# Optimization experiments

Measured on AMD Instinct MI355X. Metric: run time of the kernel, lower is better.

The kernel has to match this reference:

```python
import jax, jax.numpy as jnp
import numpy as np

B, L, H = 2, 2048, 1024
NH, HD = 16, 64          # num_heads, head_dim (NH*HD == qkv_features == H)
M = 1024                 # memory_size
SCALES = (1, 2, 4)
EPS = 1e-6


def setup_inputs() -> dict:
    key = jax.random.key(0)
    ks = jax.random.split(key, 16)
    n = lambda k, shape: (jax.random.normal(k, shape) * 0.02).astype(jnp.float32)
    return {
        "x": jax.random.normal(ks[0], (B, L, H), dtype=jnp.float32),
        "error_memory": n(ks[1], (M, H)),
        "Wq": n(ks[2], (3, H, H)), "bq": jnp.zeros((3, H), jnp.float32),
        "Wk": n(ks[3], (3, H, H)), "bk": jnp.zeros((3, H), jnp.float32),
        "Wv": n(ks[4], (3, H, H)), "bv": jnp.zeros((3, H), jnp.float32),
        "Wo": n(ks[5], (3, H, H)), "bo": jnp.zeros((3, H), jnp.float32),
        "W1": n(ks[6], (4 * H, H)), "b1": jnp.zeros((H,), jnp.float32),
        "ln_scale": jnp.ones((H,), jnp.float32),
        "ln_bias": jnp.zeros((H,), jnp.float32),
        "W2": n(ks[7], (H, H)), "b2": jnp.zeros((H,), jnp.float32),
    }


def _mha(xs, Wq, bq, Wk, bk, Wv, bv, Wo, bo):
    # flax MultiHeadDotProductAttention (self-attention, deterministic)
    Bs, S, _ = xs.shape
    q = (xs @ Wq + bq).reshape(Bs, S, NH, HD)
    k = (xs @ Wk + bk).reshape(Bs, S, NH, HD)
    v = (xs @ Wv + bv).reshape(Bs, S, NH, HD)
    att = jax.nn.softmax(
        jnp.einsum('bqhd,bkhd->bhqk', q, k) / np.sqrt(HD).astype(np.float32),
        axis=-1)
    ctx = jnp.einsum('bhqk,bkhd->bqhd', att, v).reshape(Bs, S, NH * HD)
    return ctx @ Wo + bo


def reference(x, error_memory, Wq, bq, Wk, bk, Wv, bv, Wo, bo,
              W1, b1, ln_scale, ln_bias, W2, b2):
    # multi-scale self-attention error scores
    scores = []
    for i, s in enumerate(SCALES):
        sx = x.reshape(B, L // s, s, H).mean(axis=2)
        scores.append(_mha(sx, Wq[i], bq[i], Wk[i], bk[i], Wv[i], bv[i], Wo[i], bo[i]))
    error_features = jnp.concatenate(
        [jnp.repeat(sc, s, axis=1)[:, :L, :] for sc, s in zip(scores, SCALES)],
        axis=-1)  # [B, L, 3H]

    # memory similarity softmax (detect_errors) + memory readback
    sim = jnp.einsum('blh,mh->blm', x, error_memory) / jnp.sqrt(jnp.float32(H))
    memory_weights = jax.nn.softmax(sim, axis=-1)          # [B, L, M]
    memory_context = jnp.einsum('blm,mh->blh', memory_weights, error_memory)

    cf = jnp.concatenate([error_features, memory_context], axis=-1) @ W1 + b1
    mu = cf.mean(axis=-1, keepdims=True)
    var = jnp.mean((cf - mu) ** 2, axis=-1, keepdims=True)
    cf = (cf - mu) / jnp.sqrt(var + EPS) * ln_scale + ln_bias
    cf = jax.nn.relu(cf)

    error_gate = jax.nn.sigmoid(x @ W2 + b2)
    confidence = error_gate.mean(axis=-1, keepdims=True)
    scale = jnp.sqrt(1.0 / (H * confidence + EPS))
    corrected = x + scale * error_gate * cf
    return corrected, error_gate
```

## Files before the change

kernel.cpp:

```cpp
#include <hip/hip_runtime.h>
#include <stdint.h>


#define MiBc ((size_t)1 << 20)

using s16x8 = __attribute__((ext_vector_type(8))) short;
using s16x4 = __attribute__((ext_vector_type(4))) short;
using u16x4 = __attribute__((ext_vector_type(4))) unsigned short;
using f32x4 = __attribute__((ext_vector_type(4))) float;

__device__ __forceinline__ uint16_t f2bf(float f) {
  uint32_t u = __float_as_uint(f);
  return (uint16_t)((u + 0x7fffu + ((u >> 16) & 1u)) >> 16);
}

__device__ __forceinline__ float fexp2(float x) {
  return __builtin_amdgcn_exp2f(x);
}

__device__ __forceinline__ void load_lds16(const uint16_t* g, uint16_t* l) {
  __builtin_amdgcn_global_load_lds(
      (const __attribute__((address_space(1))) void*)(const void*)g,
      (__attribute__((address_space(3))) void*)(void*)l, 16, 0, 0);
}

struct TD { const float* in; uint16_t* out; };
struct TD14 { TD d[14]; };

__global__ __launch_bounds__(256) void k_transpose(TD14 ds, int R, int C) {
  const float* in = ds.d[blockIdx.y].in;
  uint16_t* out = ds.d[blockIdx.y].out;
  const int nTC = C >> 5;
  const int bi = blockIdx.x / nTC, bj = blockIdx.x % nTC;
  __shared__ float t[32][33];
  const int tx = threadIdx.x & 31, ty = threadIdx.x >> 5;
#pragma unroll
  for (int p = 0; p < 4; ++p) {
    int r = bi * 32 + ty + p * 8;
    t[ty + p * 8][tx] = in[(size_t)r * C + bj * 32 + tx];
  }
  __syncthreads();
#pragma unroll
  for (int p = 0; p < 4; ++p) {
    int c = bj * 32 + ty + p * 8;
    out[(size_t)c * R + bi * 32 + tx] = f2bf(t[tx][ty + p * 8]);
  }
}

__global__ __launch_bounds__(256) void k_f2bf4(const float* __restrict__ in,
                                               uint16_t* __restrict__ out) {
  int i = (blockIdx.x * 256 + threadIdx.x) * 4;
  float4 v = *(const float4*)(in + i);
  u16x4 o = {f2bf(v.x), f2bf(v.y), f2bf(v.z), f2bf(v.w)};
  *(u16x4*)(out + i) = o;
}

__global__ __launch_bounds__(256) void k_biaspack(const float* __restrict__ bq,
                                                  const float* __restrict__ bk,
                                                  const float* __restrict__ bv,
                                                  float* __restrict__ dst) {
  int g = blockIdx.x * 256 + threadIdx.x;
  int i = g / 3072, j = g - i * 3072;
  const float* src = (j < 1024)   ? bq + i * 1024 + j
                     : (j < 2048) ? bk + i * 1024 + (j - 1024)
                                  : bv + i * 1024 + (j - 2048);
  dst[g] = *src;
}

__global__ __launch_bounds__(256) void k_down(const float* __restrict__ x,
                                              uint16_t* __restrict__ x1,
                                              uint16_t* __restrict__ x2,
                                              uint16_t* __restrict__ x4) {
  int g = blockIdx.x * 256 + threadIdx.x;
  int c = g & 1023;
  int l4 = (g >> 10) & 511;
  int b = g >> 19;
  const float* xp = x + (size_t)(b * 2048 + l4 * 4) * 1024 + c;
  float a0 = xp[0], a1 = xp[1024], a2 = xp[2048], a3 = xp[3072];
  size_t r1 = (size_t)(b * 2048 + l4 * 4) * 1024 + c;
  x1[r1] = f2bf(a0);
  x1[r1 + 1024] = f2bf(a1);
  x1[r1 + 2048] = f2bf(a2);
  x1[r1 + 3072] = f2bf(a3);
  size_t r2 = (size_t)(b * 1024 + l4 * 2) * 1024 + c;
  x2[r2] = f2bf(0.5f * (a0 + a1));
  x2[r2 + 1024] = f2bf(0.5f * (a2 + a3));
  x4[(size_t)(b * 512 + l4) * 1024 + c] = f2bf(0.25f * (a0 + a1 + a2 + a3));
}

__global__ __launch_bounds__(256) void k_gemm(
    const uint16_t* __restrict__ A, const uint16_t* __restrict__ BT,
    const float* __restrict__ bias, void* __restrict__ C, int M, int N, int K,
    int ldc, float scale, float qscale, int qcols, int out_bf16) {
  __shared__ __align__(16) uint16_t Al[128 * 32];
  __shared__ __align__(16) uint16_t Bl[128 * 32];
  const int tid = threadIdx.x;
  const int wave = tid >> 6, lane = tid & 63;
  const int wr = wave >> 1, wc = wave & 1;
  const int lr = lane & 15, lg = lane >> 4;
  const int bM = blockIdx.y * 128, bN = blockIdx.x * 128;
  (void)M; (void)N;

  f32x4 acc[4][4] = {};

  for (int k0 = 0; k0 < K; k0 += 32) {
    __syncthreads();
#pragma unroll
    for (int j = 0; j < 2; ++j) {
      int ck = wave * 2 + j;
      int p = ck * 64 + lane;
      int row = p >> 2, kq = p & 3;
      load_lds16(A + (size_t)(bM + row) * K + k0 + kq * 8, &Al[ck * 512]);
      load_lds16(BT + (size_t)(bN + row) * K + k0 + kq * 8, &Bl[ck * 512]);
    }
    __syncthreads();
    s16x8 af[4], bfr[4];
#pragma unroll
    for (int i = 0; i < 4; ++i)
      af[i] = *(const s16x8*)&Al[(wr * 64 + i * 16 + lr) * 32 + lg * 8];
#pragma unroll
    for (int i = 0; i < 4; ++i)
      bfr[i] = *(const s16x8*)&Bl[(wc * 64 + i * 16 + lr) * 32 + lg * 8];
#pragma unroll
    for (int i = 0; i < 4; ++i)
#pragma unroll
      for (int jn = 0; jn < 4; ++jn)
        acc[i][jn] = __builtin_amdgcn_mfma_f32_16x16x32_bf16(
            af[i], bfr[jn], acc[i][jn], 0, 0, 0);
  }

#pragma unroll
  for (int i = 0; i < 4; ++i) {
    int rg = bM + wr * 64 + i * 16 + lg * 4;
#pragma unroll
    for (int jn = 0; jn < 4; ++jn) {
      int cg = bN + wc * 64 + jn * 16 + lr;
      float bv = bias ? bias[cg] : 0.f;
      float post = (cg < qcols) ? qscale : 1.f;
#pragma unroll
      for (int r = 0; r < 4; ++r) {
        float v = (acc[i][jn][r] * scale + bv) * post;
        if (out_bf16)
          ((uint16_t*)C)[(size_t)(rg + r) * ldc + cg] = f2bf(v);
        else
          ((float*)C)[(size_t)(rg + r) * ldc + cg] = v;
      }
    }
  }
}

__global__ __launch_bounds__(256) void k_vtrans(const uint16_t* __restrict__ v,
                                                uint16_t* __restrict__ vt,
                                                int S, int ld) {
  const int nKT = S >> 6;
  const int bh = blockIdx.x / nKT, kt = blockIdx.x % nKT;
  const int b = bh >> 4, h = bh & 15;
  __shared__ uint16_t t[64][65];
  for (int i = threadIdx.x; i < 4096; i += 256) {
    int kk = i >> 6, dd = i & 63;
    t[dd][kk] = v[(size_t)(b * S + kt * 64 + kk) * ld + h * 64 + dd];
  }
  __syncthreads();
  for (int i = threadIdx.x; i < 4096; i += 256) {
    int dd = i >> 6, kk = i & 63;
    vt[((size_t)(bh * 64) + dd) * S + kt * 64 + kk] = t[dd][kk];
  }
}

__global__ __launch_bounds__(256) void k_attn(const uint16_t* __restrict__ qkv,
                                              const uint16_t* __restrict__ vt,
                                              uint16_t* __restrict__ ctx,
                                              int S) {
  const int wid = blockIdx.x * 4 + (threadIdx.x >> 6);
  const int lane = threadIdx.x & 63;
  const int nQB = S >> 5;
  const int qb = wid % nQB;
  const int bh = wid / nQB;
  const int h = bh & 15, b = bh >> 4;
  const int lr = lane & 15, lg = lane >> 4;

  const uint16_t* qp =
      qkv + (size_t)(b * S + qb * 32 + lr) * 3072 + h * 64 + lg * 8;
  s16x8 qf0[2], qf1[2];
  qf0[0] = *(const s16x8*)qp;
  qf1[0] = *(const s16x8*)(qp + 32);
  qf0[1] = *(const s16x8*)(qp + 16 * 3072);
  qf1[1] = *(const s16x8*)(qp + 16 * 3072 + 32);
  const uint16_t* kbase =
      qkv + (size_t)(b * S) * 3072 + 1024 + h * 64 + lg * 8;
  const uint16_t* vbase = vt + (size_t)(bh * 64) * S + lg * 4;

  f32x4 acc[2][4] = {};
  float mS[2] = {-1e30f, -1e30f};
  float lS[2] = {0.f, 0.f};

#define LOADK(T, K0, K1)                                               \
  {                                                                    \
    const uint16_t* kp = kbase + (size_t)((T)*16 + lr) * 3072;         \
    K0 = *(const s16x8*)kp;                                            \
    K1 = *(const s16x8*)(kp + 32);                                     \
  }
#define LOADV(T, VF)                                                   \
  {                                                                    \
    _Pragma("unroll") for (int c = 0; c < 4; ++c) VF[c] =              \
        *(const s16x4*)(vbase + (size_t)(c * 16 + lr) * S + (T)*16);   \
  }

  auto compute = [&](s16x8 K0, s16x8 K1, const s16x4 (&VF)[4]) {
#pragma unroll
    for (int f = 0; f < 2; ++f) {
      f32x4 st = {};
      st = __builtin_amdgcn_mfma_f32_16x16x32_bf16(K0, qf0[f], st, 0, 0, 0);
      st = __builtin_amdgcn_mfma_f32_16x16x32_bf16(K1, qf1[f], st, 0, 0, 0);
      float tmax = fmaxf(fmaxf(st[0], st[1]), fmaxf(st[2], st[3]));
      tmax = fmaxf(tmax, __shfl_xor(tmax, 16));
      tmax = fmaxf(tmax, __shfl_xor(tmax, 32));
      if (!__all(tmax <= mS[f])) {
        float mn = fmaxf(mS[f], tmax);
        float fac = fexp2(mS[f] - mn);
        mS[f] = mn;
        lS[f] *= fac;
#pragma unroll
        for (int c = 0; c < 4; ++c) acc[f][c] *= fac;
      }
      float p0 = fexp2(st[0] - mS[f]), p1 = fexp2(st[1] - mS[f]);
      float p2 = fexp2(st[2] - mS[f]), p3 = fexp2(st[3] - mS[f]);
      lS[f] += (p0 + p1) + (p2 + p3);
      s16x4 pb;
      pb[0] = (short)f2bf(p0);
      pb[1] = (short)f2bf(p1);
      pb[2] = (short)f2bf(p2);
      pb[3] = (short)f2bf(p3);
#pragma unroll
      for (int c = 0; c < 4; ++c)
        acc[f][c] = __builtin_amdgcn_mfma_f32_16x16x16bf16_1k(VF[c], pb,
                                                              acc[f][c], 0, 0, 0);
    }
  };

  s16x8 ka0, ka1, kb0, kb1;
  s16x4 va[4], vb[4];
  const int nT = S >> 4;
  LOADK(0, ka0, ka1);
  LOADV(0, va);
  LOADK(1, kb0, kb1);
  LOADV(1, vb);
  for (int t = 0; t < nT; t += 2) {
    compute(ka0, ka1, va);
    if (t + 2 < nT) { LOADK(t + 2, ka0, ka1); LOADV(t + 2, va); }
    compute(kb0, kb1, vb);
    if (t + 3 < nT) { LOADK(t + 3, kb0, kb1); LOADV(t + 3, vb); }
  }
#undef LOADK
#undef LOADV

#pragma unroll
  for (int f = 0; f < 2; ++f) {
    float l = lS[f];
    l += __shfl_xor(l, 16);
    l += __shfl_xor(l, 32);
    const float inv = 1.f / l;
    uint16_t* crow =
        ctx + (size_t)(b * S + qb * 32 + f * 16 + lr) * 1024 + h * 64;
#pragma unroll
    for (int c = 0; c < 4; ++c) {
      u16x4 o;
#pragma unroll
      for (int r = 0; r < 4; ++r) o[r] = f2bf(acc[f][c][r] * inv);
      *(u16x4*)(crow + c * 16 + lg * 4) = o;
    }
  }
}

__global__ __launch_bounds__(256) void k_softmax(const float* __restrict__ sim,
                                                 uint16_t* __restrict__ w) {
  __shared__ float red[4];
  const int row = blockIdx.x, t = threadIdx.x;
  const size_t base = (size_t)row * 1024 + t * 4;
  float4 v = *(const float4*)(sim + base);
  float mx = fmaxf(fmaxf(v.x, v.y), fmaxf(v.z, v.w));
#pragma unroll
  for (int o = 32; o > 0; o >>= 1) mx = fmaxf(mx, __shfl_xor(mx, o));
  if ((t & 63) == 0) red[t >> 6] = mx;
  __syncthreads();
  mx = fmaxf(fmaxf(red[0], red[1]), fmaxf(red[2], red[3]));
  __syncthreads();
  float p0 = __expf(v.x - mx), p1 = __expf(v.y - mx);
  float p2 = __expf(v.z - mx), p3 = __expf(v.w - mx);
  float s = p0 + p1 + p2 + p3;
#pragma unroll
  for (int o = 32; o > 0; o >>= 1) s += __shfl_xor(s, o);
  if ((t & 63) == 0) red[t >> 6] = s;
  __syncthreads();
  s = red[0] + red[1] + red[2] + red[3];
  float inv = 1.f / s;
  u16x4 o = {f2bf(p0 * inv), f2bf(p1 * inv), f2bf(p2 * inv), f2bf(p3 * inv)};
  *(u16x4*)(w + base) = o;
}

__global__ __launch_bounds__(256) void k_upsample(const uint16_t* __restrict__ s2,
                                                  const uint16_t* __restrict__ s4,
                                                  uint16_t* __restrict__ acf) {
  int g = blockIdx.x * 256 + threadIdx.x;
  int cg = g & 255;
  int row = g >> 8;
  int b = row >> 11, l = row & 2047;
  int c = cg * 8;
  const uint16_t* src =
      (c < 1024) ? s2 + (size_t)(b * 1024 + (l >> 1)) * 1024 + c
                 : s4 + (size_t)(b * 512 + (l >> 2)) * 1024 + (c - 1024);
  *(s16x8*)(acf + (size_t)row * 4096 + 1024 + c) = *(const s16x8*)src;
}

__global__ __launch_bounds__(256) void k_final(
    const float* __restrict__ cf, const float* __restrict__ gl,
    const float* __restrict__ x, const float* __restrict__ lns,
    const float* __restrict__ lnb, float* __restrict__ out) {
  __shared__ float red[4];
  const int row = blockIdx.x, t = threadIdx.x;
  const size_t base = (size_t)row * 1024 + t * 4;
  float4 cv = *(const float4*)(cf + base);
  float4 gv = *(const float4*)(gl + base);
  float g0 = 1.f / (1.f + __expf(-gv.x));
  float g1 = 1.f / (1.f + __expf(-gv.y));
  float g2 = 1.f / (1.f + __expf(-gv.z));
  float g3 = 1.f / (1.f + __expf(-gv.w));

  auto bsum = [&](float v) -> float {
#pragma unroll
    for (int o = 32; o > 0; o >>= 1) v += __shfl_xor(v, o);
    if ((t & 63) == 0) red[t >> 6] = v;
    __syncthreads();
    float r = red[0] + red[1] + red[2] + red[3];
    __syncthreads();
    return r;
  };
  float mu = bsum(cv.x + cv.y + cv.z + cv.w) * (1.f / 1024.f);
  float conf = bsum(g0 + g1 + g2 + g3) * (1.f / 1024.f);
  float d0 = cv.x - mu, d1 = cv.y - mu, d2 = cv.z - mu, d3 = cv.w - mu;
  float var = bsum(d0 * d0 + d1 * d1 + d2 * d2 + d3 * d3) * (1.f / 1024.f);
  float rstd = rsqrtf(var + 1e-6f);
  float4 ls = *(const float4*)(lns + t * 4);
  float4 lb = *(const float4*)(lnb + t * 4);
  float y0 = fmaxf(d0 * rstd * ls.x + lb.x, 0.f);
  float y1 = fmaxf(d1 * rstd * ls.y + lb.y, 0.f);
  float y2 = fmaxf(d2 * rstd * ls.z + lb.z, 0.f);
  float y3 = fmaxf(d3 * rstd * ls.w + lb.w, 0.f);
  float sc = sqrtf(1.f / (1024.f * conf + 1e-6f));
  float4 xv = *(const float4*)(x + base);
  float4 o1 = {xv.x + sc * g0 * y0, xv.y + sc * g1 * y1, xv.z + sc * g2 * y2,
               xv.w + sc * g3 * y3};
  *(float4*)(out + base) = o1;
  float4 o2 = {g0, g1, g2, g3};
  *(float4*)(out + 4194304 + base) = o2;
}

static constexpr size_t OFF_QKVT = 0;
static constexpr size_t OFF_WOT = 18 * MiBc;
static constexpr size_t OFF_W1T = 24 * MiBc;
static constexpr size_t OFF_W2T = 32 * MiBc;
static constexpr size_t OFF_EMB = 34 * MiBc;
static constexpr size_t OFF_EMT = 36 * MiBc;
static constexpr size_t OFF_XB1 = 38 * MiBc;
static constexpr size_t OFF_XB2 = 46 * MiBc;
static constexpr size_t OFF_XB4 = 50 * MiBc;
static constexpr size_t OFF_QKV = 52 * MiBc;
static constexpr size_t OFF_VT  = 76 * MiBc;
static constexpr size_t OFF_CTX = 84 * MiBc;
static constexpr size_t OFF_S2  = 92 * MiBc;
static constexpr size_t OFF_S4  = 96 * MiBc;
static constexpr size_t OFF_ACF = 98 * MiBc;
static constexpr size_t OFF_SIM = 130 * MiBc;
static constexpr size_t OFF_WSM = 146 * MiBc;
static constexpr size_t OFF_CF  = 154 * MiBc;
static constexpr size_t OFF_BQKV = 170 * MiBc;
static constexpr size_t WS_NEED = 186 * MiBc;

static constexpr float QSC = 0.125f * 1.44269504f;

extern "C" void kernel_launch(void* const* d_in, const int* in_sizes, int n_in,
                              void* d_out, int out_size, void* d_ws,
                              size_t ws_size, hipStream_t stream) {
  (void)in_sizes; (void)n_in; (void)out_size;
  const float* x  = (const float*)d_in[0];
  const float* em = (const float*)d_in[1];
  const float* Wq = (const float*)d_in[2];
  const float* bq = (const float*)d_in[3];
  const float* Wk = (const float*)d_in[4];
  const float* bk = (const float*)d_in[5];
  const float* Wv = (const float*)d_in[6];
  const float* bv = (const float*)d_in[7];
  const float* Wo = (const float*)d_in[8];
  const float* bo = (const float*)d_in[9];
  const float* W1 = (const float*)d_in[10];
  const float* b1 = (const float*)d_in[11];
  const float* lns = (const float*)d_in[12];
  const float* lnb = (const float*)d_in[13];
  const float* W2 = (const float*)d_in[14];
  const float* b2 = (const float*)d_in[15];
  float* out = (float*)d_out;

  if (ws_size < WS_NEED) {
    hipMemsetAsync(d_out, 0x7f, 4, stream);
    return;
  }
  uint8_t* w8 = (uint8_t*)d_ws;
  auto U16 = [&](size_t off) { return (uint16_t*)(w8 + off); };
  uint16_t* QKVT = U16(OFF_QKVT);
  uint16_t* WOT = U16(OFF_WOT);
  uint16_t* W1T = U16(OFF_W1T);
  uint16_t* W2T = U16(OFF_W2T);
  uint16_t* EMB = U16(OFF_EMB);
  uint16_t* EMT = U16(OFF_EMT);
  uint16_t* XB1 = U16(OFF_XB1);
  uint16_t* XB2 = U16(OFF_XB2);
  uint16_t* XB4 = U16(OFF_XB4);
  uint16_t* QKVb = U16(OFF_QKV);
  uint16_t* VTb = U16(OFF_VT);
  uint16_t* CTX = U16(OFF_CTX);
  uint16_t* S2b = U16(OFF_S2);
  uint16_t* S4b = U16(OFF_S4);
  uint16_t* ACF = U16(OFF_ACF);
  float* SIM = (float*)(w8 + OFF_SIM);
  uint16_t* WSM = U16(OFF_WSM);
  float* CF = (float*)(w8 + OFF_CF);
  float* BQKV = (float*)(w8 + OFF_BQKV);
  float* GL = out + 4194304;

  const size_t MM = 1024 * 1024;
  const size_t SC3 = 3 * MM;

  TD14 td{};
  for (int i = 0; i < 3; ++i) {
    td.d[i]     = {Wq + (size_t)i * MM, QKVT + (size_t)i * SC3};
    td.d[3 + i] = {Wk + (size_t)i * MM, QKVT + (size_t)i * SC3 + MM};
    td.d[6 + i] = {Wv + (size_t)i * MM, QKVT + (size_t)i * SC3 + 2 * MM};
    td.d[9 + i] = {Wo + (size_t)i * MM, WOT + (size_t)i * MM};
  }
  td.d[12] = {W2, W2T};
  td.d[13] = {em, EMT};
  k_transpose<<<dim3(1024, 14), 256, 0, stream>>>(td, 1024, 1024);
  TD14 t1{};
  t1.d[0] = {W1, W1T};
  k_transpose<<<dim3(4096, 1), 256, 0, stream>>>(t1, 4096, 1024);
  k_f2bf4<<<dim3(1024), 256, 0, stream>>>(em, EMB);
  k_biaspack<<<dim3(36), 256, 0, stream>>>(bq, bk, bv, BQKV);
  k_down<<<dim3(4096), 256, 0, stream>>>(x, XB1, XB2, XB4);

  for (int i = 0; i < 3; ++i) {
    const int S = 2048 >> i;
    const int R = 2 * S;
    const uint16_t* xb = (i == 0) ? XB1 : (i == 1) ? XB2 : XB4;
    k_gemm<<<dim3(24, R / 128), 256, 0, stream>>>(
        xb, QKVT + (size_t)i * SC3, BQKV + i * 3072, QKVb, R, 3072, 1024, 3072,
        1.f, QSC, 1024, 1);
    k_vtrans<<<dim3(32 * (S / 64)), 256, 0, stream>>>(QKVb + 2048, VTb, S, 3072);
    k_attn<<<dim3(S / 4), 256, 0, stream>>>(QKVb, VTb, CTX, S);
    dim3 gg(8, R / 128);
    if (i == 0)
      k_gemm<<<gg, 256, 0, stream>>>(CTX, WOT, bo, ACF, R, 1024, 1024, 4096,
                                     1.f, 1.f, 0, 1);
    else if (i == 1)
      k_gemm<<<gg, 256, 0, stream>>>(CTX, WOT + MM, bo + 1024, S2b, R, 1024,
                                     1024, 1024, 1.f, 1.f, 0, 1);
    else
      k_gemm<<<gg, 256, 0, stream>>>(CTX, WOT + 2 * MM, bo + 2048, S4b, R, 1024,
                                     1024, 1024, 1.f, 1.f, 0, 1);
  }

  k_gemm<<<dim3(8, 32), 256, 0, stream>>>(XB1, EMB, nullptr, SIM, 4096, 1024,
                                          1024, 1024, 0.03125f, 1.f, 0, 0);
  k_softmax<<<dim3(4096), 256, 0, stream>>>(SIM, WSM);
  k_gemm<<<dim3(8, 32), 256, 0, stream>>>(WSM, EMT, nullptr, ACF + 3072, 4096,
                                          1024, 1024, 4096, 1.f, 1.f, 0, 1);
  k_upsample<<<dim3(4096), 256, 0, stream>>>(S2b, S4b, ACF);

  k_gemm<<<dim3(8, 32), 256, 0, stream>>>(ACF, W1T, b1, CF, 4096, 1024, 4096,
                                          1024, 1.f, 1.f, 0, 0);
  k_gemm<<<dim3(8, 32), 256, 0, stream>>>(XB1, W2T, b2, GL, 4096, 1024, 1024,
                                          1024, 1.f, 1.f, 0, 0);
  k_final<<<dim3(4096), 256, 0, stream>>>(CF, GL, x, lns, lnb, out);
}
```

Baseline: 818.2 us.

## Split attention key range across four waves per block with LDS merge

Each block now owns a single 32-query tile, and its four waves each handle an interleaved quarter of the key tiles. Partial max, sum and accumulators go into shared memory and are merged with a log-sum-exp rescale, each wave writing 16 output columns. The grid grows fourfold, so there are more waves in flight and each wave runs a shorter serial loop over keys. The cost is extra shared memory, two barriers per fragment, and the merge arithmetic.

```diff
diff --git a/kernel.cpp b/kernel.cpp
--- a/kernel.cpp
+++ b/kernel.cpp
@@ -171,11 +171,13 @@
                                               const uint16_t* __restrict__ vt,
                                               uint16_t* __restrict__ ctx,
                                               int S) {
-  const int wid = blockIdx.x * 4 + (threadIdx.x >> 6);
+  __shared__ float2 mlb[4][64];
+  __shared__ __align__(16) float accb[4][64][4][4];
   const int lane = threadIdx.x & 63;
+  const int wv = threadIdx.x >> 6;
   const int nQB = S >> 5;
-  const int qb = wid % nQB;
-  const int bh = wid / nQB;
+  const int bh = blockIdx.x / nQB;
+  const int qb = blockIdx.x % nQB;
   const int h = bh & 15, b = bh >> 4;
   const int lr = lane & 15, lg = lane >> 4;
 
@@ -241,34 +243,47 @@
   s16x8 ka0, ka1, kb0, kb1;
   s16x4 va[4], vb[4];
   const int nT = S >> 4;
-  LOADK(0, ka0, ka1);
-  LOADV(0, va);
-  LOADK(1, kb0, kb1);
-  LOADV(1, vb);
-  for (int t = 0; t < nT; t += 2) {
+  LOADK(wv, ka0, ka1);
+  LOADV(wv, va);
+  LOADK(wv + 4, kb0, kb1);
+  LOADV(wv + 4, vb);
+  for (int t = wv; t < nT; t += 8) {
     compute(ka0, ka1, va);
-    if (t + 2 < nT) { LOADK(t + 2, ka0, ka1); LOADV(t + 2, va); }
+    if (t + 8 < nT) { LOADK(t + 8, ka0, ka1); LOADV(t + 8, va); }
     compute(kb0, kb1, vb);
-    if (t + 3 < nT) { LOADK(t + 3, kb0, kb1); LOADV(t + 3, vb); }
+    if (t + 12 < nT) { LOADK(t + 12, kb0, kb1); LOADV(t + 12, vb); }
   }
 #undef LOADK
 #undef LOADV
 
 #pragma unroll
   for (int f = 0; f < 2; ++f) {
-    float l = lS[f];
-    l += __shfl_xor(l, 16);
-    l += __shfl_xor(l, 32);
-    const float inv = 1.f / l;
+    float lred = lS[f];
+    lred += __shfl_xor(lred, 16);
+    lred += __shfl_xor(lred, 32);
+    mlb[wv][lane] = {mS[f], lred};
+#pragma unroll
+    for (int c = 0; c < 4; ++c)
+      *(f32x4*)&accb[wv][lane][c][0] = acc[f][c];
+    __syncthreads();
+    float2 ml0 = mlb[0][lane], ml1 = mlb[1][lane];
+    float2 ml2 = mlb[2][lane], ml3 = mlb[3][lane];
+    float M = fmaxf(fmaxf(ml0.x, ml1.x), fmaxf(ml2.x, ml3.x));
+    float s0 = fexp2(ml0.x - M), s1 = fexp2(ml1.x - M);
+    float s2 = fexp2(ml2.x - M), s3 = fexp2(ml3.x - M);
+    float L = s0 * ml0.y + s1 * ml1.y + s2 * ml2.y + s3 * ml3.y;
+    f32x4 O = *(const f32x4*)&accb[0][lane][wv][0] * s0;
+    O += *(const f32x4*)&accb[1][lane][wv][0] * s1;
+    O += *(const f32x4*)&accb[2][lane][wv][0] * s2;
+    O += *(const f32x4*)&accb[3][lane][wv][0] * s3;
+    const float inv = 1.f / L;
     uint16_t* crow =
         ctx + (size_t)(b * S + qb * 32 + f * 16 + lr) * 1024 + h * 64;
-#pragma unroll
-    for (int c = 0; c < 4; ++c) {
-      u16x4 o;
-#pragma unroll
-      for (int r = 0; r < 4; ++r) o[r] = f2bf(acc[f][c][r] * inv);
-      *(u16x4*)(crow + c * 16 + lg * 4) = o;
-    }
+    u16x4 o;
+#pragma unroll
+    for (int r = 0; r < 4; ++r) o[r] = f2bf(O[r] * inv);
+    *(u16x4*)(crow + wv * 16 + lg * 4) = o;
+    __syncthreads();
   }
 }
 
@@ -455,7 +470,7 @@
         xb, QKVT + (size_t)i * SC3, BQKV + i * 3072, QKVb, R, 3072, 1024, 3072,
         1.f, QSC, 1024, 1);
     k_vtrans<<<dim3(32 * (S / 64)), 256, 0, stream>>>(QKVb + 2048, VTb, S, 3072);
-    k_attn<<<dim3(S / 4), 256, 0, stream>>>(QKVb, VTb, CTX, S);
+    k_attn<<<dim3(32 * (S / 32)), 256, 0, stream>>>(QKVb, VTb, CTX, S);
     dim3 gg(8, R / 128);
     if (i == 0)
       k_gemm<<<gg, 256, 0, stream>>>(CTX, WOT, bo, ACF, R, 1024, 1024, 4096,
```

Measured after the change: 808.7 us. About the same (-1.2%).

## Share K/V tiles across waves via swizzled LDS in attention kernel

Applied to the files above, without the earlier changes.

Restructures the attention kernel so each 256-thread block covers 128 query rows of one head. The four waves now cooperatively stage 64-key K and V^T tiles into XOR-swizzled LDS with async global-to-LDS loads, instead of each wave streaming K/V straight from global memory into registers. This cuts redundant global/L2 traffic by sharing each K/V tile across four waves. In exchange it adds two barriers per tile and drops the register double-buffered prefetch, so load latency is no longer overlapped with compute within a wave.

```diff
diff --git a/kernel.cpp b/kernel.cpp
--- a/kernel.cpp
+++ b/kernel.cpp
@@ -171,88 +171,95 @@
                                               const uint16_t* __restrict__ vt,
                                               uint16_t* __restrict__ ctx,
                                               int S) {
-  const int wid = blockIdx.x * 4 + (threadIdx.x >> 6);
+  __shared__ __align__(16) uint16_t Kl[64 * 64];
+  __shared__ __align__(16) uint16_t Vl[64 * 64];
   const int lane = threadIdx.x & 63;
-  const int nQB = S >> 5;
-  const int qb = wid % nQB;
-  const int bh = wid / nQB;
+  const int wv = threadIdx.x >> 6;
+  const int nQB = S >> 7;
+  const int bh = blockIdx.x / nQB;
+  const int qb = blockIdx.x % nQB;
   const int h = bh & 15, b = bh >> 4;
   const int lr = lane & 15, lg = lane >> 4;
 
+  const int qrow0 = qb * 128 + wv * 32;
   const uint16_t* qp =
-      qkv + (size_t)(b * S + qb * 32 + lr) * 3072 + h * 64 + lg * 8;
+      qkv + (size_t)(b * S + qrow0 + lr) * 3072 + h * 64 + lg * 8;
   s16x8 qf0[2], qf1[2];
   qf0[0] = *(const s16x8*)qp;
   qf1[0] = *(const s16x8*)(qp + 32);
   qf0[1] = *(const s16x8*)(qp + 16 * 3072);
   qf1[1] = *(const s16x8*)(qp + 16 * 3072 + 32);
-  const uint16_t* kbase =
-      qkv + (size_t)(b * S) * 3072 + 1024 + h * 64 + lg * 8;
-  const uint16_t* vbase = vt + (size_t)(bh * 64) * S + lg * 4;
+  const uint16_t* kg = qkv + (size_t)(b * S) * 3072 + 1024 + h * 64;
+  const uint16_t* vg = vt + (size_t)(bh * 64) * S;
 
   f32x4 acc[2][4] = {};
   float mS[2] = {-1e30f, -1e30f};
   float lS[2] = {0.f, 0.f};
 
-#define LOADK(T, K0, K1)                                               \
-  {                                                                    \
-    const uint16_t* kp = kbase + (size_t)((T)*16 + lr) * 3072;         \
-    K0 = *(const s16x8*)kp;                                            \
-    K1 = *(const s16x8*)(kp + 32);                                     \
-  }
-#define LOADV(T, VF)                                                   \
-  {                                                                    \
-    _Pragma("unroll") for (int c = 0; c < 4; ++c) VF[c] =              \
-        *(const s16x4*)(vbase + (size_t)(c * 16 + lr) * S + (T)*16);   \
-  }
-
-  auto compute = [&](s16x8 K0, s16x8 K1, const s16x4 (&VF)[4]) {
-#pragma unroll
-    for (int f = 0; f < 2; ++f) {
-      f32x4 st = {};
-      st = __builtin_amdgcn_mfma_f32_16x16x32_bf16(K0, qf0[f], st, 0, 0, 0);
-      st = __builtin_amdgcn_mfma_f32_16x16x32_bf16(K1, qf1[f], st, 0, 0, 0);
-      float tmax = fmaxf(fmaxf(st[0], st[1]), fmaxf(st[2], st[3]));
-      tmax = fmaxf(tmax, __shfl_xor(tmax, 16));
-      tmax = fmaxf(tmax, __shfl_xor(tmax, 32));
-      if (!__all(tmax <= mS[f])) {
-        float mn = fmaxf(mS[f], tmax);
-        float fac = fexp2(mS[f] - mn);
-        mS[f] = mn;
-        lS[f] *= fac;
-#pragma unroll
-        for (int c = 0; c < 4; ++c) acc[f][c] *= fac;
+  const int srl = lane >> 3;
+  const int ssl = (lane & 7) ^ (srl & 7);
+
+  const int nKV = S >> 6;
+  for (int blk = 0; blk < nKV; ++blk) {
+    __syncthreads();
+#pragma unroll
+    for (int j = 0; j < 4; ++j) {
+      int ck = wv * 4 + j;
+      int rl = ((ck & 7) << 3) + srl;
+      if (ck < 8)
+        load_lds16(kg + (size_t)(blk * 64 + rl) * 3072 + ssl * 8,
+                   &Kl[(ck & 7) * 512]);
+      else
+        load_lds16(vg + (size_t)rl * S + blk * 64 + ssl * 8,
+                   &Vl[(ck & 7) * 512]);
+    }
+    __syncthreads();
+
+#pragma unroll
+    for (int kt = 0; kt < 4; ++kt) {
+      const int r = kt * 16 + lr;
+      const int sw = r & 7;
+      s16x8 K0 = *(const s16x8*)&Kl[r * 64 + ((lg ^ sw) << 3)];
+      s16x8 K1 = *(const s16x8*)&Kl[r * 64 + (((lg + 4) ^ sw) << 3)];
+      s16x4 vf[4];
+#pragma unroll
+      for (int c = 0; c < 4; ++c) {
+        int d = c * 16 + lr;
+        int s16 = (kt << 1) | (lg >> 1);
+        vf[c] = *(const s16x4*)&Vl[d * 64 + (((s16 ^ (d & 7)) << 3) |
+                                             ((lg & 1) << 2))];
       }
-      float p0 = fexp2(st[0] - mS[f]), p1 = fexp2(st[1] - mS[f]);
-      float p2 = fexp2(st[2] - mS[f]), p3 = fexp2(st[3] - mS[f]);
-      lS[f] += (p0 + p1) + (p2 + p3);
-      s16x4 pb;
-      pb[0] = (short)f2bf(p0);
-      pb[1] = (short)f2bf(p1);
-      pb[2] = (short)f2bf(p2);
-      pb[3] = (short)f2bf(p3);
-#pragma unroll
-      for (int c = 0; c < 4; ++c)
-        acc[f][c] = __builtin_amdgcn_mfma_f32_16x16x16bf16_1k(VF[c], pb,
-                                                              acc[f][c], 0, 0, 0);
+#pragma unroll
+      for (int f = 0; f < 2; ++f) {
+        f32x4 st = {};
+        st = __builtin_amdgcn_mfma_f32_16x16x32_bf16(K0, qf0[f], st, 0, 0, 0);
+        st = __builtin_amdgcn_mfma_f32_16x16x32_bf16(K1, qf1[f], st, 0, 0, 0);
+        float tmax = fmaxf(fmaxf(st[0], st[1]), fmaxf(st[2], st[3]));
+        tmax = fmaxf(tmax, __shfl_xor(tmax, 16));
+        tmax = fmaxf(tmax, __shfl_xor(tmax, 32));
+        if (!__all(tmax <= mS[f])) {
+          float mn = fmaxf(mS[f], tmax);
+          float fac = fexp2(mS[f] - mn);
+          mS[f] = mn;
+          lS[f] *= fac;
+#pragma unroll
+          for (int c = 0; c < 4; ++c) acc[f][c] *= fac;
+        }
+        float p0 = fexp2(st[0] - mS[f]), p1 = fexp2(st[1] - mS[f]);
+        float p2 = fexp2(st[2] - mS[f]), p3 = fexp2(st[3] - mS[f]);
+        lS[f] += (p0 + p1) + (p2 + p3);
+        s16x4 pb;
+        pb[0] = (short)f2bf(p0);
+        pb[1] = (short)f2bf(p1);
+        pb[2] = (short)f2bf(p2);
+        pb[3] = (short)f2bf(p3);
+#pragma unroll
+        for (int c = 0; c < 4; ++c)
+          acc[f][c] = __builtin_amdgcn_mfma_f32_16x16x16bf16_1k(
+              vf[c], pb, acc[f][c], 0, 0, 0);
+      }
     }
-  };
-
-  s16x8 ka0, ka1, kb0, kb1;
-  s16x4 va[4], vb[4];
-  const int nT = S >> 4;
-  LOADK(0, ka0, ka1);
-  LOADV(0, va);
-  LOADK(1, kb0, kb1);
-  LOADV(1, vb);
-  for (int t = 0; t < nT; t += 2) {
-    compute(ka0, ka1, va);
-    if (t + 2 < nT) { LOADK(t + 2, ka0, ka1); LOADV(t + 2, va); }
-    compute(kb0, kb1, vb);
-    if (t + 3 < nT) { LOADK(t + 3, kb0, kb1); LOADV(t + 3, vb); }
-  }
-#undef LOADK
-#undef LOADV
+  }
 
 #pragma unroll
   for (int f = 0; f < 2; ++f) {
@@ -261,7 +268,7 @@
     l += __shfl_xor(l, 32);
     const float inv = 1.f / l;
     uint16_t* crow =
-        ctx + (size_t)(b * S + qb * 32 + f * 16 + lr) * 1024 + h * 64;
+        ctx + (size_t)(b * S + qrow0 + f * 16 + lr) * 1024 + h * 64;
 #pragma unroll
     for (int c = 0; c < 4; ++c) {
       u16x4 o;
@@ -455,7 +462,7 @@
         xb, QKVT + (size_t)i * SC3, BQKV + i * 3072, QKVb, R, 3072, 1024, 3072,
         1.f, QSC, 1024, 1);
     k_vtrans<<<dim3(32 * (S / 64)), 256, 0, stream>>>(QKVb + 2048, VTb, S, 3072);
-    k_attn<<<dim3(S / 4), 256, 0, stream>>>(QKVb, VTb, CTX, S);
+    k_attn<<<dim3(32 * (S / 128)), 256, 0, stream>>>(QKVb, VTb, CTX, S);
     dim3 gg(8, R / 128);
     if (i == 0)
       k_gemm<<<gg, 256, 0, stream>>>(CTX, WOT, bo, ACF, R, 1024, 1024, 4096,
```

After: 730.0 us. -10.8%, faster.
